# Optimization experiments

Measured on AMD Instinct MI355X. Metric: run time of the kernel, lower is better.

## Reference

```python
import jax, jax.numpy as jnp
import numpy as np

B, S, DM, H = 2, 2048, 1024, 16        # dim_model = d_model//2 = 1024
WINDOW, DILATION, N_GLOBAL = 513, 2, 32
HD = DM // H
NEG = -1e9


def build_mask(n, window_size, dilation, global_idx):
    # dilated local window: |i-j| <= (window//2)*dilation and (i-j) % dilation == 0
    i = jnp.arange(n)[:, None]
    j = jnp.arange(n)[None, :]
    d = j - i
    half = window_size // 2
    local = (jnp.abs(d) <= half * dilation) & (jnp.mod(d, dilation) == 0)
    g = jnp.zeros((n,), bool).at[global_idx].set(True)
    # symmetric global token mask: global rows and columns fully attend
    return local | g[:, None] | g[None, :]


def setup_inputs() -> dict:
    key = jax.random.key(0)
    ks = jax.random.split(key, 9)
    std = 0.02
    inp = {
        "q": jax.random.normal(ks[0], (B, S, DM), jnp.float32),
        "k": jax.random.normal(ks[1], (B, S, DM), jnp.float32),
        "v": jax.random.normal(ks[2], (B, S, DM), jnp.float32),
        "Wq": jax.random.normal(ks[3], (DM, DM), jnp.float32) * std,
        "Wk": jax.random.normal(ks[4], (DM, DM), jnp.float32) * std,
        "Wv": jax.random.normal(ks[5], (DM, DM), jnp.float32) * std,
        "Wo": jax.random.normal(ks[6], (DM, DM), jnp.float32) * std,
        "bq": jnp.zeros((DM,), jnp.float32),
        "bk": jnp.zeros((DM,), jnp.float32),
        "bv": jnp.zeros((DM,), jnp.float32),
        "bo": jnp.zeros((DM,), jnp.float32),
        "global_idx": jax.random.randint(ks[7], (N_GLOBAL,), 0, S, jnp.int64)
        if jax.config.jax_enable_x64 else jax.random.randint(ks[7], (N_GLOBAL,), 0, S, jnp.int32),
    }
    return inp


def reference(q, k, v, Wq, Wk, Wv, Wo, bq, bk, bv, bo, global_idx):
    def split(x):  # [B,S,DM] -> [B,H,S,HD]
        return x.reshape(B, S, H, HD).transpose(0, 2, 1, 3)

    qh = split(q @ Wq.T + bq)
    kh = split(k @ Wk.T + bk)
    vh = split(v @ Wv.T + bv)

    scores = jnp.einsum("bhqd,bhkd->bhqk", qh, kh) / jnp.sqrt(jnp.asarray(HD, qh.dtype))
    mask = build_mask(S, WINDOW, DILATION, global_idx)  # [S,S] bool
    scores = jnp.where(mask[None, None], scores, NEG)
    attn = jax.nn.softmax(scores, axis=-1)
    out = jnp.einsum("bhqk,bhkd->bhqd", attn, vh)
    out = out.transpose(0, 2, 1, 3).reshape(B, S, DM)
    return out @ Wo.T + bo
```

## Files before the change

### kernel.cpp

```cpp
#include <hip/hip_runtime.h>
#include <hip/hip_bf16.h>
#include <math.h>

#define BB 2
#define SS 2048
#define DMM 1024
#define HH 16
#define HDD 64
#define NGLOB 32
#define MM 4096
#define SCALE2 0.18033688f

typedef __attribute__((ext_vector_type(8))) short short8;
typedef __attribute__((ext_vector_type(4))) float float4v;

__device__ __forceinline__ short f2bf(float f) {
    union { float f; unsigned u; } x; x.f = f;
    unsigned r = (x.u + 0x7fffu + ((x.u >> 16) & 1u)) >> 16;
    return (short)r;
}

#define ASYNC16(gp, lp) __builtin_amdgcn_global_load_lds( \
    (__attribute__((address_space(1))) void*)(gp), \
    (__attribute__((address_space(3))) void*)(lp), 16, 0, 0)

#define VSL(dim, key) ((dim) * 40 + (((((key) >> 3) ^ (((dim) >> 3) & 3)) << 3) | ((key) & 7)))

__global__ void setup_globals(const int* __restrict__ gidx, int* __restrict__ g,
                              int* __restrict__ glist, int* __restrict__ gcount) {
    int t = threadIdx.x;
    for (int i = t; i < SS; i += 256) g[i] = 0;
    if (t == 0) *gcount = 0;
    __syncthreads();
    if (t < NGLOB) {
        int j = gidx[t];
        if (j >= 0 && j < SS) g[j] = 1;
    }
    __syncthreads();
    for (int j = t; j < SS; j += 256) {
        if (g[j]) {
            int p = atomicAdd(gcount, 1);
            glist[p] = j;
        }
    }
}

__global__ __launch_bounds__(256)
void convert_all(const float* __restrict__ q, const float* __restrict__ k,
                 const float* __restrict__ v,
                 const float* __restrict__ w0, const float* __restrict__ w1,
                 const float* __restrict__ w2, const float* __restrict__ w3,
                 short* __restrict__ abf, short* __restrict__ wbf) {
    int z = blockIdx.y;
    const float* src;
    short* dst;
    size_t n;
    if (z < 3) {
        src = (z == 0) ? q : (z == 1) ? k : v;
        dst = abf + (size_t)z * ((size_t)MM * DMM);
        n = (size_t)MM * DMM;
    } else {
        int y = z - 3;
        src = (y == 0) ? w0 : (y == 1) ? w1 : (y == 2) ? w2 : w3;
        dst = wbf + (size_t)y * ((size_t)DMM * DMM);
        n = (size_t)DMM * DMM;
    }
    size_t i = ((size_t)blockIdx.x * 256 + threadIdx.x) * 8;
    if (i >= n) return;
    float4 a = *(const float4*)(src + i);
    float4 b = *(const float4*)(src + i + 4);
    short8 s;
    s[0]=f2bf(a.x); s[1]=f2bf(a.y); s[2]=f2bf(a.z); s[3]=f2bf(a.w);
    s[4]=f2bf(b.x); s[5]=f2bf(b.y); s[6]=f2bf(b.z); s[7]=f2bf(b.w);
    *(short8*)(dst + i) = s;
}

template<int OBF, int HEADSPLIT>
__global__ __launch_bounds__(256)
void gemm128(const short* __restrict__ Abase, const short* __restrict__ Wbase,
             const float* __restrict__ b0, const float* __restrict__ b1,
             const float* __restrict__ b2,
             void* __restrict__ O0p, void* __restrict__ O1p, void* __restrict__ O2p) {
    __shared__ short As[2][128 * 32];
    __shared__ short Ws[2][128 * 32];

    int t = threadIdx.x;
    int z = blockIdx.y;
    const short* A    = Abase + (size_t)z * ((size_t)MM * DMM);
    const short* W    = Wbase + (size_t)z * ((size_t)DMM * DMM);
    const float* bias = (z == 0) ? b0 : (z == 1) ? b1 : b2;
    void* outp        = (z == 0) ? O0p : (z == 1) ? O1p : O2p;

    int bid = blockIdx.x;
    int xcd = bid & 7, loc = bid >> 3;
    int nblk = loc & 7, mloc = loc >> 3;
    int m0 = (xcd * 4 + mloc) * 128;
    int n0 = nblk * 128;

    int lane = t & 63, w = t >> 6;
    int quad = lane >> 4, col = lane & 15;
    int wr = (w & 1) * 64;
    int wc = (w >> 1) * 64;

    float4v acc[4][4];
    #pragma unroll
    for (int i = 0; i < 4; i++)
        #pragma unroll
        for (int j = 0; j < 4; j++) acc[i][j] = (float4v){0, 0, 0, 0};

    int rowA = t >> 2,  kcA = (t & 3) * 8;
    const short* Ap = A + (size_t)(m0 + rowA) * DMM + kcA;
    const short* Wp = W + (size_t)(n0 + rowA) * DMM + kcA;

    #define STAGE(bf, tt) do { int kk = (tt) * 32; \
        ASYNC16(Ap + kk,                      &As[bf][t * 8]); \
        ASYNC16(Ap + 64 * (size_t)DMM + kk,   &As[bf][2048 + t * 8]); \
        ASYNC16(Wp + kk,                      &Ws[bf][t * 8]); \
        ASYNC16(Wp + 64 * (size_t)DMM + kk,   &Ws[bf][2048 + t * 8]); \
    } while (0)

    STAGE(0, 0);
    asm volatile("s_waitcnt vmcnt(0)" ::: "memory");
    __builtin_amdgcn_s_barrier();

    for (int it = 0; it < 32; it++) {
        int cur = it & 1;
        if (it + 1 < 32) STAGE(cur ^ 1, it + 1);

        short8 aF[4], bF[4];
        #pragma unroll
        for (int i = 0; i < 4; i++)
            aF[i] = *(short8*)&As[cur][(wr + 16 * i + col) * 32 + quad * 8];
        #pragma unroll
        for (int j = 0; j < 4; j++)
            bF[j] = *(short8*)&Ws[cur][(wc + 16 * j + col) * 32 + quad * 8];

        __builtin_amdgcn_s_setprio(1);
        #pragma unroll
        for (int i = 0; i < 4; i++)
            #pragma unroll
            for (int j = 0; j < 4; j++)
                acc[i][j] = __builtin_amdgcn_mfma_f32_16x16x32_bf16(aF[i], bF[j], acc[i][j], 0, 0, 0);
        __builtin_amdgcn_s_setprio(0);

        asm volatile("s_waitcnt vmcnt(0)" ::: "memory");
        __builtin_amdgcn_s_barrier();
    }
    #undef STAGE

    #pragma unroll
    for (int i = 0; i < 4; i++) {
        #pragma unroll
        for (int j = 0; j < 4; j++) {
            int n = n0 + wc + 16 * j + col;
            float bn = bias[n];
            #pragma unroll
            for (int r = 0; r < 4; r++) {
                int m = m0 + wr + 16 * i + quad * 4 + r;
                float val = acc[i][j][r] + bn;
                size_t idx;
                if (HEADSPLIT) {
                    int b = m >> 11;
                    int s = m & 2047;
                    int h = n >> 6;
                    int hd = n & 63;
                    idx = (((size_t)b * HH + h) * SS + s) * HDD + hd;
                } else {
                    idx = (size_t)m * DMM + n;
                }
                if (OBF) ((short*)outp)[idx] = f2bf(val);
                else     ((float*)outp)[idx] = val;
            }
        }
    }
}

__global__ __launch_bounds__(256)
void band_attn(const short* __restrict__ qh, const short* __restrict__ kh,
               const short* __restrict__ vh, const int* __restrict__ glist,
               const int* __restrict__ gcount, short* __restrict__ ao) {
    __shared__ short Qs[64 * 72];
    __shared__ short Ks[32 * 72];
    __shared__ short Vt[64 * 40];
    __shared__ short Ps[4 * 16 * 40];
    __shared__ int   gjs[32];

    int t = threadIdx.x;
    int bid = blockIdx.x;
    int xcd = bid & 7, idx = bid >> 3;
    int gl  = idx >> 4;
    int qt  = idx & 15;
    int gid = xcd * 8 + gl;
    int z   = gid >> 4;
    int h   = gid & 15;
    int b = z >> 1, p = z & 1;
    int qq0 = qt * 64;
    int nG = *gcount;

    const short* Qb = qh + ((size_t)(b * HH + h) * SS) * HDD;
    const short* Kb = kh + ((size_t)(b * HH + h) * SS) * HDD;
    const short* Vb = vh + ((size_t)(b * HH + h) * SS) * HDD;

    int row8 = t >> 3;
    int dim8 = (t & 7) * 8;

    #pragma unroll
    for (int rr = 0; rr < 2; rr++) {
        int row = rr * 32 + row8;
        int i = 2 * (qq0 + row) + p;
        short8 qv = *(const short8*)(Qb + (size_t)i * HDD + dim8);
        *(short8*)&Qs[row * 72 + dim8] = qv;
    }
    if (t < 32) gjs[t] = (t < nG) ? glist[t] : -1000000;
    __syncthreads();

    int lane = t & 63, w = t >> 6;
    int quad = lane >> 4, col = lane & 15;

    short8 qf0 = *(short8*)&Qs[(16 * w + col) * 72 + quad * 8];
    short8 qf1 = *(short8*)&Qs[(16 * w + col) * 72 + 32 + quad * 8];

    float4v O0 = {0,0,0,0}, O1 = {0,0,0,0}, O2 = {0,0,0,0}, O3 = {0,0,0,0};
    float lst[4] = {0.f, 0.f, 0.f, 0.f};

    short8 kvP, vvP, kvN, vvN;
    {
        int srow = 2 * (qq0 - 256 + row8) + p;
        srow = srow < 0 ? 0 : (srow > SS - 1 ? SS - 1 : srow);
        kvP = *(const short8*)(Kb + (size_t)srow * HDD + dim8);
        vvP = *(const short8*)(Vb + (size_t)srow * HDD + dim8);
    }

    for (int c = 0; c < 19; c++) {
        __syncthreads();
        *(short8*)&Ks[row8 * 72 + dim8] = kvP;
        #pragma unroll
        for (int j = 0; j < 8; j++) {
            int d = dim8 + j;
            Vt[VSL(d, row8)] = vvP[j];
        }
        if (c < 18) {
            int cn = c + 1;
            int ch0n = qq0 - 256 + cn * 32;
            int srow;
            if (cn < 18) srow = 2 * (ch0n + row8) + p;
            else         srow = (row8 < nG) ? gjs[row8] : 0;
            srow = srow < 0 ? 0 : (srow > SS - 1 ? SS - 1 : srow);
            kvN = *(const short8*)(Kb + (size_t)srow * HDD + dim8);
            vvN = *(const short8*)(Vb + (size_t)srow * HDD + dim8);
        }
        __syncthreads();

        int ch0 = qq0 - 256 + c * 32;

        short8 kA0 = *(short8*)&Ks[col * 72 + quad * 8];
        short8 kA1 = *(short8*)&Ks[col * 72 + 32 + quad * 8];
        short8 kB0 = *(short8*)&Ks[(16 + col) * 72 + quad * 8];
        short8 kB1 = *(short8*)&Ks[(16 + col) * 72 + 32 + quad * 8];
        float4v sA = {0,0,0,0}, sB = {0,0,0,0};
        sA = __builtin_amdgcn_mfma_f32_16x16x32_bf16(qf0, kA0, sA, 0, 0, 0);
        sA = __builtin_amdgcn_mfma_f32_16x16x32_bf16(qf1, kA1, sA, 0, 0, 0);
        sB = __builtin_amdgcn_mfma_f32_16x16x32_bf16(qf0, kB0, sB, 0, 0, 0);
        sB = __builtin_amdgcn_mfma_f32_16x16x32_bf16(qf1, kB1, sB, 0, 0, 0);

        if (c < 18) {
            int nlo = -ch0;
            int nhi = 1023 - ch0;
            #pragma unroll
            for (int r = 0; r < 4; r++) {
                int qq = qq0 + 16 * w + quad * 4 + r;
                int u  = qq - ch0;
                int lo = max(u - 256, nlo);
                int hi = min(u + 256, nhi);
                bool vA = (col >= lo) && (col <= hi);
                bool vB = (col + 16 >= lo) && (col + 16 <= hi);
                float pa = vA ? exp2f(sA[r] * SCALE2) : 0.f;
                float pb = vB ? exp2f(sB[r] * SCALE2) : 0.f;
                lst[r] += pa + pb;
                Ps[(w * 16 + quad * 4 + r) * 40 + col]      = f2bf(pa);
                Ps[(w * 16 + quad * 4 + r) * 40 + col + 16] = f2bf(pb);
            }
        } else {
            #pragma unroll
            for (int r = 0; r < 4; r++) {
                int qq = qq0 + 16 * w + quad * 4 + r;
                int i = 2 * qq + p;
                int jA = gjs[col], jB = gjs[col + 16];
                int dA = jA - i, dB = jB - i;
                int aA = dA < 0 ? -dA : dA;
                int aB = dB < 0 ? -dB : dB;
                bool vA = (jA >= 0) && !((aA <= 512) && ((dA & 1) == 0));
                bool vB = (jB >= 0) && !((aB <= 512) && ((dB & 1) == 0));
                float pa = vA ? exp2f(sA[r] * SCALE2) : 0.f;
                float pb = vB ? exp2f(sB[r] * SCALE2) : 0.f;
                lst[r] += pa + pb;
                Ps[(w * 16 + quad * 4 + r) * 40 + col]      = f2bf(pa);
                Ps[(w * 16 + quad * 4 + r) * 40 + col + 16] = f2bf(pb);
            }
        }
        asm volatile("s_waitcnt lgkmcnt(0)" ::: "memory");

        short8 pf  = *(short8*)&Ps[(w * 16 + col) * 40 + quad * 8];
        short8 vf0 = *(short8*)&Vt[(col) * 40 + ((quad ^ ((col >> 3) & 3)) << 3)];
        short8 vf1 = *(short8*)&Vt[(16 + col) * 40 + ((quad ^ (((16 + col) >> 3) & 3)) << 3)];
        short8 vf2 = *(short8*)&Vt[(32 + col) * 40 + ((quad ^ (((32 + col) >> 3) & 3)) << 3)];
        short8 vf3 = *(short8*)&Vt[(48 + col) * 40 + ((quad ^ (((48 + col) >> 3) & 3)) << 3)];
        O0 = __builtin_amdgcn_mfma_f32_16x16x32_bf16(pf, vf0, O0, 0, 0, 0);
        O1 = __builtin_amdgcn_mfma_f32_16x16x32_bf16(pf, vf1, O1, 0, 0, 0);
        O2 = __builtin_amdgcn_mfma_f32_16x16x32_bf16(pf, vf2, O2, 0, 0, 0);
        O3 = __builtin_amdgcn_mfma_f32_16x16x32_bf16(pf, vf3, O3, 0, 0, 0);

        kvP = kvN; vvP = vvN;
    }

    #pragma unroll
    for (int r = 0; r < 4; r++) {
        float l = lst[r];
        #pragma unroll
        for (int mk = 1; mk < 16; mk <<= 1) l += __shfl_xor(l, mk);
        float inv = 1.0f / l;
        int q = 16 * w + quad * 4 + r;
        int i = 2 * (qq0 + q) + p;
        short* dst = ao + ((size_t)b * SS + i) * DMM + h * HDD;
        dst[col]      = f2bf(O0[r] * inv);
        dst[col + 16] = f2bf(O1[r] * inv);
        dst[col + 32] = f2bf(O2[r] * inv);
        dst[col + 48] = f2bf(O3[r] * inv);
    }
}

__global__ __launch_bounds__(256)
void global_part(const short* __restrict__ qh, const short* __restrict__ kh,
                 const short* __restrict__ vh, const int* __restrict__ glist,
                 const int* __restrict__ gcount,
                 float* __restrict__ pl, float* __restrict__ pO) {
    __shared__ short Qs[32 * 72];
    __shared__ short Ks[2][32 * 72];
    __shared__ short Vt[2][64 * 40];
    __shared__ short Ps[4 * 16 * 40];

    int t = threadIdx.x;
    int s = blockIdx.x, h = blockIdx.y, b = blockIdx.z;
    int nG = *gcount;

    const short* Qb = qh + ((size_t)(b * HH + h) * SS) * HDD;
    const short* Kb = kh + ((size_t)(b * HH + h) * SS) * HDD;
    const short* Vb = vh + ((size_t)(b * HH + h) * SS) * HDD;

    int row8 = t >> 3, dim8 = (t & 7) * 8;
    {
        int cq = row8 < nG ? row8 : 0;
        int src = glist[cq];
        short8 qv = *(const short8*)(Qb + (size_t)src * HDD + dim8);
        *(short8*)&Qs[row8 * 72 + dim8] = qv;
    }
    __syncthreads();

    int lane = t & 63, w = t >> 6;
    int quad = lane >> 4, col = lane & 15;
    int g = w >> 1, qt = w & 1;

    short8 qf0 = *(short8*)&Qs[(qt * 16 + col) * 72 + quad * 8];
    short8 qf1 = *(short8*)&Qs[(qt * 16 + col) * 72 + 32 + quad * 8];

    float4v O0 = {0,0,0,0}, O1 = {0,0,0,0}, O2 = {0,0,0,0}, O3 = {0,0,0,0};
    float lst[4] = {0.f, 0.f, 0.f, 0.f};

    int js0 = s * 256;
    for (int it = 0; it < 4; it++) {
        __syncthreads();
        int r64 = t >> 2, dimb = (t & 3) * 16;
        int j = js0 + it * 64 + r64;
        const short* kp = Kb + (size_t)j * HDD + dimb;
        const short* vp = Vb + (size_t)j * HDD + dimb;
        short8 k0 = *(const short8*)kp, k1 = *(const short8*)(kp + 8);
        short8 v0 = *(const short8*)vp, v1 = *(const short8*)(vp + 8);
        int half = r64 >> 5, r32 = r64 & 31;
        *(short8*)&Ks[half][r32 * 72 + dimb]     = k0;
        *(short8*)&Ks[half][r32 * 72 + dimb + 8] = k1;
        #pragma unroll
        for (int u = 0; u < 8; u++) {
            int d = dimb + u;
            Vt[half][VSL(d, r32)] = v0[u];
        }
        #pragma unroll
        for (int u = 0; u < 8; u++) {
            int d = dimb + 8 + u;
            Vt[half][VSL(d, r32)] = v1[u];
        }
        __syncthreads();

        short8 kA0 = *(short8*)&Ks[g][col * 72 + quad * 8];
        short8 kA1 = *(short8*)&Ks[g][col * 72 + 32 + quad * 8];
        short8 kB0 = *(short8*)&Ks[g][(16 + col) * 72 + quad * 8];
        short8 kB1 = *(short8*)&Ks[g][(16 + col) * 72 + 32 + quad * 8];
        float4v sA = {0,0,0,0}, sB = {0,0,0,0};
        sA = __builtin_amdgcn_mfma_f32_16x16x32_bf16(qf0, kA0, sA, 0, 0, 0);
        sA = __builtin_amdgcn_mfma_f32_16x16x32_bf16(qf1, kA1, sA, 0, 0, 0);
        sB = __builtin_amdgcn_mfma_f32_16x16x32_bf16(qf0, kB0, sB, 0, 0, 0);
        sB = __builtin_amdgcn_mfma_f32_16x16x32_bf16(qf1, kB1, sB, 0, 0, 0);

        #pragma unroll
        for (int r = 0; r < 4; r++) {
            float pa = exp2f(sA[r] * SCALE2);
            float pb = exp2f(sB[r] * SCALE2);
            lst[r] += pa + pb;
            Ps[(w * 16 + quad * 4 + r) * 40 + col]      = f2bf(pa);
            Ps[(w * 16 + quad * 4 + r) * 40 + col + 16] = f2bf(pb);
        }
        asm volatile("s_waitcnt lgkmcnt(0)" ::: "memory");

        short8 pf  = *(short8*)&Ps[(w * 16 + col) * 40 + quad * 8];
        short8 vf0 = *(short8*)&Vt[g][(col) * 40 + ((quad ^ ((col >> 3) & 3)) << 3)];
        short8 vf1 = *(short8*)&Vt[g][(16 + col) * 40 + ((quad ^ (((16 + col) >> 3) & 3)) << 3)];
        short8 vf2 = *(short8*)&Vt[g][(32 + col) * 40 + ((quad ^ (((32 + col) >> 3) & 3)) << 3)];
        short8 vf3 = *(short8*)&Vt[g][(48 + col) * 40 + ((quad ^ (((48 + col) >> 3) & 3)) << 3)];
        O0 = __builtin_amdgcn_mfma_f32_16x16x32_bf16(pf, vf0, O0, 0, 0, 0);
        O1 = __builtin_amdgcn_mfma_f32_16x16x32_bf16(pf, vf1, O1, 0, 0, 0);
        O2 = __builtin_amdgcn_mfma_f32_16x16x32_bf16(pf, vf2, O2, 0, 0, 0);
        O3 = __builtin_amdgcn_mfma_f32_16x16x32_bf16(pf, vf3, O3, 0, 0, 0);
    }

    int sp = s * 2 + g;
    size_t base = ((size_t)(b * HH + h) * 16 + sp) * 32;
    #pragma unroll
    for (int r = 0; r < 4; r++) {
        float l = lst[r];
        #pragma unroll
        for (int mk = 1; mk < 16; mk <<= 1) l += __shfl_xor(l, mk);
        int q = qt * 16 + quad * 4 + r;
        if (col == 0) pl[base + q] = l;
        float* Od = pO + (base + q) * 64;
        Od[col]      = O0[r];
        Od[col + 16] = O1[r];
        Od[col + 32] = O2[r];
        Od[col + 48] = O3[r];
    }
}

__global__ __launch_bounds__(256)
void global_merge(const float* __restrict__ pl, const float* __restrict__ pO,
                  const int* __restrict__ glist, const int* __restrict__ gcount,
                  short* __restrict__ ao) {
    int h = blockIdx.x, b = blockIdx.y;
    int t = threadIdx.x;
    int d = t & 63, qg = t >> 6;
    int nG = *gcount;
    size_t bh = ((size_t)(b * HH + h) * 16) * 32;

    for (int q = qg; q < nG; q += 4) {
        float L = 0.f, acc = 0.f;
        #pragma unroll
        for (int sp = 0; sp < 16; sp++) {
            L   += pl[bh + sp * 32 + q];
            acc += pO[(bh + sp * 32 + q) * 64 + d];
        }
        int i = glist[q];
        ao[((size_t)b * SS + i) * DMM + h * HDD + d] = f2bf(acc / L);
    }
}

extern "C" void kernel_launch(void* const* d_in, const int* in_sizes, int n_in,
                              void* d_out, int out_size, void* d_ws, size_t ws_size,
                              hipStream_t stream) {
    const float* q  = (const float*)d_in[0];
    const float* k  = (const float*)d_in[1];
    const float* v  = (const float*)d_in[2];
    const float* Wq = (const float*)d_in[3];
    const float* Wk = (const float*)d_in[4];
    const float* Wv = (const float*)d_in[5];
    const float* Wo = (const float*)d_in[6];
    const float* bq = (const float*)d_in[7];
    const float* bk = (const float*)d_in[8];
    const float* bv = (const float*)d_in[9];
    const float* bo = (const float*)d_in[10];
    const int* gidx = (const int*)d_in[11];
    float* out = (float*)d_out;

    const size_t NE = (size_t)BB * SS * DMM;
    const size_t WE = (size_t)DMM * DMM;
    int*   g      = (int*)d_ws;
    int*   glist  = g + SS;
    int*   gcount = glist + SS;
    short* qh     = (short*)((char*)d_ws + 32768);
    short* kh     = qh + NE;
    short* vh     = kh + NE;
    short* ao     = vh + NE;
    short* wbf    = ao + NE;
    short* wo     = wbf + 3 * WE;
    short* abf    = wbf + 4 * WE;
    float* pl     = (float*)abf;
    float* pO     = pl + 16384;

    setup_globals<<<1, 256, 0, stream>>>(gidx, g, glist, gcount);

    dim3 gc(2048, 7);
    convert_all<<<gc, 256, 0, stream>>>(q, k, v, Wq, Wk, Wv, Wo, abf, wbf);

    dim3 gq(256, 3);
    gemm128<1, 1><<<gq, 256, 0, stream>>>(abf, wbf, bq, bk, bv, qh, kh, vh);

    band_attn<<<1024, 256, 0, stream>>>(qh, kh, vh, glist, gcount, ao);

    dim3 gp(8, HH, BB);
    global_part<<<gp, 256, 0, stream>>>(qh, kh, vh, glist, gcount, pl, pO);

    dim3 gm(HH, BB);
    global_merge<<<gm, 256, 0, stream>>>(pl, pO, glist, gcount, ao);

    dim3 go(256, 1);
    gemm128<0, 0><<<go, 256, 0, stream>>>(ao, wo, bo, bo, bo, out, out, out);
}
```

Measured before the change: 234.8 us.

## Use 256x256 swizzled-LDS GEMM for QKV projection and 64-row tiles for output

The QKV projection GEMM moves from 128x128 tiles with 256 threads to 256x256 tiles with 512 threads. It uses a K-step of 64, XOR-swizzled LDS to avoid bank conflicts, and a partial vmcnt wait so the next stage's loads overlap with compute. The output projection gets a separate 64x128-tile kernel that launches 512 blocks instead of 256, to fill more CUs. The trade-off is that the larger tile uses 128KB of LDS and more accumulator registers per thread. The QKV launch also shrinks to 192 blocks, which may leave some CUs idle.

```diff
diff --git a/kernel.cpp b/kernel.cpp
--- a/kernel.cpp
+++ b/kernel.cpp
@@ -76,13 +76,13 @@
 }
 
 template<int OBF, int HEADSPLIT>
-__global__ __launch_bounds__(256)
-void gemm128(const short* __restrict__ Abase, const short* __restrict__ Wbase,
+__global__ __launch_bounds__(512, 2)
+void gemm256(const short* __restrict__ Abase, const short* __restrict__ Wbase,
              const float* __restrict__ b0, const float* __restrict__ b1,
              const float* __restrict__ b2,
              void* __restrict__ O0p, void* __restrict__ O1p, void* __restrict__ O2p) {
-    __shared__ short As[2][128 * 32];
-    __shared__ short Ws[2][128 * 32];
+    __shared__ short As[2][256 * 64];
+    __shared__ short Ws[2][256 * 64];
 
     int t = threadIdx.x;
     int z = blockIdx.y;
@@ -92,71 +92,94 @@
     void* outp        = (z == 0) ? O0p : (z == 1) ? O1p : O2p;
 
     int bid = blockIdx.x;
-    int xcd = bid & 7, loc = bid >> 3;
-    int nblk = loc & 7, mloc = loc >> 3;
-    int m0 = (xcd * 4 + mloc) * 128;
-    int n0 = nblk * 128;
+    int mt = bid & 15, nt = bid >> 4;
+    int m0 = mt * 256, n0 = nt * 256;
 
     int lane = t & 63, w = t >> 6;
     int quad = lane >> 4, col = lane & 15;
-    int wr = (w & 1) * 64;
-    int wc = (w >> 1) * 64;
-
-    float4v acc[4][4];
+    int wm = (w >> 2) * 128;
+    int wn = (w & 3) * 64;
+
+    float4v acc[8][4];
     #pragma unroll
-    for (int i = 0; i < 4; i++)
+    for (int i = 0; i < 8; i++)
         #pragma unroll
         for (int j = 0; j < 4; j++) acc[i][j] = (float4v){0, 0, 0, 0};
 
-    int rowA = t >> 2,  kcA = (t & 3) * 8;
-    const short* Ap = A + (size_t)(m0 + rowA) * DMM + kcA;
-    const short* Wp = W + (size_t)(n0 + rowA) * DMM + kcA;
-
-    #define STAGE(bf, tt) do { int kk = (tt) * 32; \
-        ASYNC16(Ap + kk,                      &As[bf][t * 8]); \
-        ASYNC16(Ap + 64 * (size_t)DMM + kk,   &As[bf][2048 + t * 8]); \
-        ASYNC16(Wp + kk,                      &Ws[bf][t * 8]); \
-        ASYNC16(Wp + 64 * (size_t)DMM + kk,   &Ws[bf][2048 + t * 8]); \
+    int srow = t >> 3;
+    int scol = ((t & 7) ^ (srow & 7)) * 8;
+    const short* Ap = A + (size_t)(m0 + srow) * DMM + scol;
+    const short* Wp = W + (size_t)(n0 + srow) * DMM + scol;
+
+    #define STAGE256(bf, tt) do { size_t kk = (size_t)(tt) * 64; \
+        ASYNC16(Ap + kk,                        &As[bf][t * 8]); \
+        ASYNC16(Ap +  64 * (size_t)DMM + kk,    &As[bf][4096  + t * 8]); \
+        ASYNC16(Ap + 128 * (size_t)DMM + kk,    &As[bf][8192  + t * 8]); \
+        ASYNC16(Ap + 192 * (size_t)DMM + kk,    &As[bf][12288 + t * 8]); \
+        ASYNC16(Wp + kk,                        &Ws[bf][t * 8]); \
+        ASYNC16(Wp +  64 * (size_t)DMM + kk,    &Ws[bf][4096  + t * 8]); \
+        ASYNC16(Wp + 128 * (size_t)DMM + kk,    &Ws[bf][8192  + t * 8]); \
+        ASYNC16(Wp + 192 * (size_t)DMM + kk,    &Ws[bf][12288 + t * 8]); \
     } while (0)
 
-    STAGE(0, 0);
-    asm volatile("s_waitcnt vmcnt(0)" ::: "memory");
-    __builtin_amdgcn_s_barrier();
-
-    for (int it = 0; it < 32; it++) {
+    int c7 = col & 7;
+
+    STAGE256(0, 0);
+
+    for (int it = 0; it < 16; it++) {
         int cur = it & 1;
-        if (it + 1 < 32) STAGE(cur ^ 1, it + 1);
-
-        short8 aF[4], bF[4];
-        #pragma unroll
-        for (int i = 0; i < 4; i++)
-            aF[i] = *(short8*)&As[cur][(wr + 16 * i + col) * 32 + quad * 8];
-        #pragma unroll
-        for (int j = 0; j < 4; j++)
-            bF[j] = *(short8*)&Ws[cur][(wc + 16 * j + col) * 32 + quad * 8];
-
-        __builtin_amdgcn_s_setprio(1);
-        #pragma unroll
-        for (int i = 0; i < 4; i++)
-            #pragma unroll
-            for (int j = 0; j < 4; j++)
-                acc[i][j] = __builtin_amdgcn_mfma_f32_16x16x32_bf16(aF[i], bF[j], acc[i][j], 0, 0, 0);
-        __builtin_amdgcn_s_setprio(0);
-
-        asm volatile("s_waitcnt vmcnt(0)" ::: "memory");
+        if (it < 15) {
+            STAGE256(cur ^ 1, it + 1);
+            asm volatile("s_waitcnt vmcnt(8)" ::: "memory");
+        } else {
+            asm volatile("s_waitcnt vmcnt(0)" ::: "memory");
+        }
         __builtin_amdgcn_s_barrier();
-    }
-    #undef STAGE
+
+        short8 bF[4][2];
+        #pragma unroll
+        for (int j = 0; j < 4; j++) {
+            int rB = (wn + 16 * j + col) * 64;
+            #pragma unroll
+            for (int ks = 0; ks < 2; ks++)
+                bF[j][ks] = *(short8*)&Ws[cur][rB + ((((ks << 2) | quad) ^ c7) << 3)];
+        }
+
+        #pragma unroll
+        for (int p = 0; p < 4; p++) {
+            if (p) __builtin_amdgcn_s_barrier();
+            short8 aF[2][2];
+            #pragma unroll
+            for (int u = 0; u < 2; u++) {
+                int rA = (wm + 16 * (2 * p + u) + col) * 64;
+                #pragma unroll
+                for (int ks = 0; ks < 2; ks++)
+                    aF[u][ks] = *(short8*)&As[cur][rA + ((((ks << 2) | quad) ^ c7) << 3)];
+            }
+            __builtin_amdgcn_s_setprio(1);
+            #pragma unroll
+            for (int ks = 0; ks < 2; ks++)
+                #pragma unroll
+                for (int u = 0; u < 2; u++)
+                    #pragma unroll
+                    for (int j = 0; j < 4; j++)
+                        acc[2 * p + u][j] = __builtin_amdgcn_mfma_f32_16x16x32_bf16(
+                            aF[u][ks], bF[j][ks], acc[2 * p + u][j], 0, 0, 0);
+            __builtin_amdgcn_s_setprio(0);
+        }
+        __builtin_amdgcn_s_barrier();
+    }
+    #undef STAGE256
 
     #pragma unroll
-    for (int i = 0; i < 4; i++) {
+    for (int i = 0; i < 8; i++) {
         #pragma unroll
         for (int j = 0; j < 4; j++) {
-            int n = n0 + wc + 16 * j + col;
+            int n = n0 + wn + 16 * j + col;
             float bn = bias[n];
             #pragma unroll
             for (int r = 0; r < 4; r++) {
-                int m = m0 + wr + 16 * i + quad * 4 + r;
+                int m = m0 + wm + 16 * i + quad * 4 + r;
                 float val = acc[i][j][r] + bn;
                 size_t idx;
                 if (HEADSPLIT) {
@@ -170,6 +193,83 @@
                 }
                 if (OBF) ((short*)outp)[idx] = f2bf(val);
                 else     ((float*)outp)[idx] = val;
+            }
+        }
+    }
+}
+
+__global__ __launch_bounds__(256)
+void gemm64p(const short* __restrict__ A, const short* __restrict__ W,
+             const float* __restrict__ bias, float* __restrict__ out) {
+    __shared__ short As[2][64 * 32];
+    __shared__ short Ws[2][128 * 32];
+
+    int t = threadIdx.x;
+    int bid = blockIdx.x;
+    int xcd = bid & 7, loc = bid >> 3;
+    int nblk = loc & 7, mloc = loc >> 3;
+    int m0 = (xcd * 8 + mloc) * 64;
+    int n0 = nblk * 128;
+
+    int lane = t & 63, w = t >> 6;
+    int quad = lane >> 4, col = lane & 15;
+    int arow0 = (w & 1) * 32;
+    int ncol0 = (w >> 1) * 64;
+
+    float4v acc[2][4];
+    #pragma unroll
+    for (int i = 0; i < 2; i++)
+        #pragma unroll
+        for (int j = 0; j < 4; j++) acc[i][j] = (float4v){0, 0, 0, 0};
+
+    const short* Apa = A + (size_t)(m0 + (t >> 2)) * DMM + (t & 3) * 8;
+    const short* Wp  = W + (size_t)(n0 + (t >> 2)) * DMM + (t & 3) * 8;
+
+    #define STAGEW(bf, tt) do { int kk = (tt) * 32; \
+        ASYNC16(Apa + kk,                     &As[bf][t * 8]); \
+        ASYNC16(Wp + kk,                      &Ws[bf][t * 8]); \
+        ASYNC16(Wp + 64 * (size_t)DMM + kk,   &Ws[bf][2048 + t * 8]); \
+    } while (0)
+
+    STAGEW(0, 0);
+    asm volatile("s_waitcnt vmcnt(0)" ::: "memory");
+    __builtin_amdgcn_s_barrier();
+
+    for (int it = 0; it < 32; it++) {
+        int cur = it & 1;
+        if (it + 1 < 32) STAGEW(cur ^ 1, it + 1);
+
+        short8 aF[2], bF[4];
+        #pragma unroll
+        for (int i = 0; i < 2; i++)
+            aF[i] = *(short8*)&As[cur][(arow0 + 16 * i + col) * 32 + quad * 8];
+        #pragma unroll
+        for (int j = 0; j < 4; j++)
+            bF[j] = *(short8*)&Ws[cur][(ncol0 + 16 * j + col) * 32 + quad * 8];
+
+        __builtin_amdgcn_s_setprio(1);
+        #pragma unroll
+        for (int i = 0; i < 2; i++)
+            #pragma unroll
+            for (int j = 0; j < 4; j++)
+                acc[i][j] = __builtin_amdgcn_mfma_f32_16x16x32_bf16(aF[i], bF[j], acc[i][j], 0, 0, 0);
+        __builtin_amdgcn_s_setprio(0);
+
+        asm volatile("s_waitcnt vmcnt(0)" ::: "memory");
+        __builtin_amdgcn_s_barrier();
+    }
+    #undef STAGEW
+
+    #pragma unroll
+    for (int i = 0; i < 2; i++) {
+        #pragma unroll
+        for (int j = 0; j < 4; j++) {
+            int n = n0 + ncol0 + 16 * j + col;
+            float bn = bias[n];
+            #pragma unroll
+            for (int r = 0; r < 4; r++) {
+                int m = m0 + arow0 + 16 * i + quad * 4 + r;
+                out[(size_t)m * DMM + n] = acc[i][j][r] + bn;
             }
         }
     }
@@ -497,8 +597,8 @@
     dim3 gc(2048, 7);
     convert_all<<<gc, 256, 0, stream>>>(q, k, v, Wq, Wk, Wv, Wo, abf, wbf);
 
-    dim3 gq(256, 3);
-    gemm128<1, 1><<<gq, 256, 0, stream>>>(abf, wbf, bq, bk, bv, qh, kh, vh);
+    dim3 gq(64, 3);
+    gemm256<1, 1><<<gq, 512, 0, stream>>>(abf, wbf, bq, bk, bv, qh, kh, vh);
 
     band_attn<<<1024, 256, 0, stream>>>(qh, kh, vh, glist, gcount, ao);
 
@@ -508,6 +608,5 @@
     dim3 gm(HH, BB);
     global_merge<<<gm, 256, 0, stream>>>(pl, pO, glist, gcount, ao);
 
-    dim3 go(256, 1);
-    gemm128<0, 0><<<go, 256, 0, stream>>>(ao, wo, bo, bo, bo, out, out, out);
-}
+    gemm64p<<<512, 256, 0, stream>>>(ao, wo, bo, out);
+}
```

After: 232.3 us. Within noise of the previous version (-1.1%).
